# Kernel tuning notes

Measured on AMD Instinct MI355X. Metric: run time of the kernel, lower is better.

Reference implementation:

```python
import jax, jax.numpy as jnp
import numpy as np

B, S, DMODEL = 1, 2048, 4096
H, HKV, DH = 32, 8, 128
LTAB, RBKT = 20, 128
NEG = -1e9


def rotate_half(x):
    x1, x2 = x[..., : x.shape[-1] // 2], x[..., x.shape[-1] // 2:]
    return jnp.concatenate((-x2, x1), axis=-1)


def setup_inputs() -> dict:
    key = jax.random.key(0)
    ks = jax.random.split(key, 12)
    inp = {
        "hidden_states": jax.random.normal(ks[0], (B, S, DMODEL), jnp.float32),
        "cos": jax.random.uniform(ks[1], (B, S, DH), jnp.float32),
        "sin": jax.random.uniform(ks[2], (B, S, DH), jnp.float32),
        "q_probs": jax.random.uniform(ks[3], (B, H, LTAB, RBKT), jnp.float32),
        "v_norm": jax.random.uniform(ks[4], (B, H, S), jnp.float32),
        "allowed": jnp.ones((B, H, S), dtype=bool),
        "k_hard": jax.random.randint(ks[5], (B, H, LTAB, S), 0, RBKT, jnp.int32),
        "Wq": jax.random.normal(ks[6], (DMODEL, H * DH), jnp.float32) * 0.02,
        "Wk": jax.random.normal(ks[7], (DMODEL, HKV * DH), jnp.float32) * 0.02,
        "Wv": jax.random.normal(ks[8], (DMODEL, HKV * DH), jnp.float32) * 0.02,
        "Wo": jax.random.normal(ks[9], (H * DH, DMODEL), jnp.float32) * 0.02,
        "sink": 4,
        "window": 128,
        "M": 256,
    }
    return inp


def _sparse_key_mask(q_probs, v_norm, allowed, k_hard, sink, window, M):
    """Faithful jax version of build_sparse_list_decode, returned as a boolean
    allowed-key mask [B, H, T] (equivalent to scattering sparse_list)."""
    Bm, Hm, _, T = k_hard.shape
    # soft-hash collision score: sum over tables of q bucket prob at key's bucket,
    # weighted by value-norm history, restricted to allowed keys.
    coll = jnp.take_along_axis(q_probs, k_hard.astype(jnp.int32), axis=-1).sum(axis=2)  # [B,H,T]
    scores = jnp.where(allowed, coll * v_norm, -jnp.inf)
    M_eff = min(M, T)
    mask = jnp.zeros((Bm, Hm, T), dtype=bool)
    if M_eff > 0:
        heavy_idx = jax.lax.top_k(scores, M_eff)[1]  # [B,H,M]
        b_ix = jnp.arange(Bm)[:, None, None]
        h_ix = jnp.arange(Hm)[None, :, None]
        mask = mask.at[b_ix, h_ix, heavy_idx].set(True)
    sink = max(0, min(sink, T))
    window = max(0, min(window, T))
    if sink > 0:
        mask = mask.at[:, :, :sink].set(True)
    if window > 0:
        win_start = max(T - window, sink)
        if win_start < T:
            mask = mask.at[:, :, win_start:].set(True)
    if sink == 0 and window == 0:
        mask = mask.at[:, :, T - 1].set(True)
    return mask & allowed


def reference(hidden_states, cos, sin, q_probs, v_norm, allowed, k_hard,
              Wq, Wk, Wv, Wo, sink, window, M):
    Bx, Sx, _ = hidden_states.shape
    scaling = DH ** -0.5
    q = (hidden_states @ Wq).reshape(Bx, Sx, H, DH).transpose(0, 2, 1, 3)   # [B,H,S,Dh]
    k = (hidden_states @ Wk).reshape(Bx, Sx, HKV, DH).transpose(0, 2, 1, 3)  # [B,Hkv,S,Dh]
    v = (hidden_states @ Wv).reshape(Bx, Sx, HKV, DH).transpose(0, 2, 1, 3)
    # RoPE (unsqueeze_dim=1)
    c, s = cos[:, None, :, :], sin[:, None, :, :]
    q = q * c + rotate_half(q) * s
    k = k * c + rotate_half(k) * s
    # repeat_kv for GQA
    n_rep = H // HKV
    k = jnp.repeat(k, n_rep, axis=1)
    v = jnp.repeat(v, n_rep, axis=1)
    # sparse heavy-hitter + sink + window key mask (no_grad in the original)
    key_mask = _sparse_key_mask(q_probs, v_norm, allowed, k_hard, sink, window, M)  # [B,H,S]
    causal = jnp.tril(jnp.ones((Sx, Sx), dtype=bool))
    allow = causal[None, None] & key_mask[:, :, None, :]  # [B,H,S,S]
    scores = jnp.einsum('bhqd,bhkd->bhqk', q, k) * scaling
    attn = jax.nn.softmax(jnp.where(allow, scores, NEG), axis=-1)
    out = jnp.einsum('bhqk,bhkd->bhqd', attn, v)
    out = out.transpose(0, 2, 1, 3).reshape(Bx, Sx, H * DH)
    return out @ Wo
```

## Files before the change

### kernel.cpp

```cpp
#include <hip/hip_runtime.h>
#include <hip/hip_bf16.h>
#include <cstdint>
#include <cstddef>

namespace {

constexpr int S_LEN = 2048;
constexpr int DM    = 4096;
constexpr int NH    = 32;
constexpr int NKV   = 8;
constexpr int DH    = 128;
constexpr int LTAB  = 20;
constexpr int RBKT  = 128;
constexpr int NQKV  = NH * DH + 2 * NKV * DH;
constexpr int KOFF  = NH * DH;
constexpr int VOFF  = NH * DH + NKV * DH;

typedef short s16x8 __attribute__((ext_vector_type(8)));
typedef float f32x4 __attribute__((ext_vector_type(4)));
typedef unsigned long long u64;
struct u64x2 { u64 x, y; };

__device__ inline short bf16s(float f) {
  __hip_bfloat16 b = __float2bfloat16(f);
  return (short)*reinterpret_cast<unsigned short*>(&b);
}
__device__ inline float s2f(short s) {
  unsigned short u = (unsigned short)s;
  return __bfloat162float(*reinterpret_cast<__hip_bfloat16*>(&u));
}

__global__ __launch_bounds__(256) void prep_kernel(
    const float* __restrict__ hidden, const float* __restrict__ Wq,
    const float* __restrict__ Wk, const float* __restrict__ Wv,
    const float* __restrict__ Wo, __hip_bfloat16* __restrict__ hbf,
    __hip_bfloat16* __restrict__ WqkvT, __hip_bfloat16* __restrict__ WoT,
    const float* __restrict__ q_probs, const float* __restrict__ v_norm,
    const int* __restrict__ allowed, const int* __restrict__ k_hard,
    const int* __restrict__ sinkp, const int* __restrict__ winp,
    const int* __restrict__ Mp, int* __restrict__ sel_idx, int* __restrict__ sel_cnt) {
  __shared__ float tile[64][65];
  __shared__ u64 keys[S_LEN];
  __shared__ int waveTot[4];
  const int b = blockIdx.x, tid = threadIdx.x;
  if (b < 32) {
    const int h = b;
    const int lane = tid & 63, wv4 = tid >> 6;
    const int t0 = tid * 8;
    float cs[8] = {0.f, 0.f, 0.f, 0.f, 0.f, 0.f, 0.f, 0.f};
#pragma unroll
    for (int l = 0; l < LTAB; ++l) {
      const int* kb = &k_hard[(size_t)(h * LTAB + l) * S_LEN + t0];
      const int4 ka = *reinterpret_cast<const int4*>(kb);
      const int4 kc = *reinterpret_cast<const int4*>(kb + 4);
      const float* qp = &q_probs[(h * LTAB + l) * RBKT];
      cs[0] += qp[ka.x]; cs[1] += qp[ka.y]; cs[2] += qp[ka.z]; cs[3] += qp[ka.w];
      cs[4] += qp[kc.x]; cs[5] += qp[kc.y]; cs[6] += qp[kc.z]; cs[7] += qp[kc.w];
    }
    const int4 alA = *reinterpret_cast<const int4*>(&allowed[h * S_LEN + t0]);
    const int4 alB = *reinterpret_cast<const int4*>(&allowed[h * S_LEN + t0 + 4]);
    const float4 vnA = *reinterpret_cast<const float4*>(&v_norm[h * S_LEN + t0]);
    const float4 vnB = *reinterpret_cast<const float4*>(&v_norm[h * S_LEN + t0 + 4]);
    const int al[8] = {alA.x, alA.y, alA.z, alA.w, alB.x, alB.y, alB.z, alB.w};
    const float vn[8] = {vnA.x, vnA.y, vnA.z, vnA.w, vnB.x, vnB.y, vnB.z, vnB.w};
    auto mkkey = [](float s, int t) -> u64 {
      unsigned m = __float_as_uint(s);
      m = (m & 0x80000000u) ? ~m : (m | 0x80000000u);
      return ((u64)m << 11) | (u64)(S_LEN - 1 - t);
    };
    u64 kk[8];
#pragma unroll
    for (int c = 0; c < 8; ++c) {
      const float sc = al[c] ? cs[c] * vn[c] : -INFINITY;
      kk[c] = mkkey(sc, t0 + c);
      keys[t0 + c] = kk[c];
    }
    __syncthreads();
    int rk[8] = {0, 0, 0, 0, 0, 0, 0, 0};
#pragma unroll 4
    for (int u = 0; u < S_LEN; u += 2) {
      const u64x2 kv = *reinterpret_cast<const u64x2*>(&keys[u]);
#pragma unroll
      for (int c = 0; c < 8; ++c) rk[c] += (kv.x > kk[c]) + (kv.y > kk[c]);
    }
    const int Mv = min(Mp[0], S_LEN);
    int sv = sinkp[0];
    sv = sv < 0 ? 0 : (sv > S_LEN ? S_LEN : sv);
    int wvv = winp[0];
    wvv = wvv < 0 ? 0 : (wvv > S_LEN ? S_LEN : wvv);
    int wstart = S_LEN - wvv;
    if (wstart < sv) wstart = sv;
    bool sel[8];
    int cnt = 0;
#pragma unroll
    for (int c = 0; c < 8; ++c) {
      const int t = t0 + c;
      bool s = rk[c] < Mv;
      if (t < sv) s = true;
      if (wvv > 0 && t >= wstart) s = true;
      if (sv == 0 && wvv == 0 && t == S_LEN - 1) s = true;
      s = s && (al[c] != 0);
      sel[c] = s;
      cnt += s ? 1 : 0;
    }
    int inc = cnt;
#pragma unroll
    for (int off = 1; off < 64; off <<= 1) {
      int n = __shfl_up(inc, off);
      if (lane >= off) inc += n;
    }
    if (lane == 63) waveTot[wv4] = inc;
    __syncthreads();
    int wbase = 0;
    for (int w = 0; w < wv4; ++w) wbase += waveTot[w];
    int pos = wbase + inc - cnt;
    if (tid == 0) sel_cnt[h] = waveTot[0] + waveTot[1] + waveTot[2] + waveTot[3];
#pragma unroll
    for (int c = 0; c < 8; ++c)
      if (sel[c]) sel_idx[h * S_LEN + pos++] = t0 + c;
    return;
  }
  if (b < 32 + 2048) {
    const size_t base = (size_t)(b - 32) * 1024;
#pragma unroll
    for (int it = 0; it < 4; ++it) {
      const size_t i = base + it * 256 + tid;
      float4 v = reinterpret_cast<const float4*>(hidden)[i];
      ushort4 o;
      o.x = (unsigned short)bf16s(v.x);
      o.y = (unsigned short)bf16s(v.y);
      o.z = (unsigned short)bf16s(v.z);
      o.w = (unsigned short)bf16s(v.w);
      reinterpret_cast<ushort4*>(hbf)[i] = o;
    }
    return;
  }
  const float* W;
  __hip_bfloat16* Wt;
  int N, bx, by;
  int t = b - 2080;
  if (t < 4096) {
    W = Wq; Wt = WqkvT; N = DM; bx = t & 63; by = t >> 6;
  } else if (t < 5120) {
    t -= 4096; W = Wk; Wt = WqkvT + (size_t)KOFF * DM; N = NKV * DH; bx = t & 15; by = t >> 4;
  } else if (t < 6144) {
    t -= 5120; W = Wv; Wt = WqkvT + (size_t)VOFF * DM; N = NKV * DH; bx = t & 15; by = t >> 4;
  } else {
    t -= 6144; W = Wo; Wt = WoT; N = DM; bx = t & 63; by = t >> 6;
  }
  const int K = DM;
  const int kb = by * 64, nb = bx * 64;
  const int r0 = tid >> 4, c4 = (tid & 15) * 4;
#pragma unroll
  for (int it = 0; it < 4; ++it) {
    const int r = r0 + it * 16;
    float4 v = *reinterpret_cast<const float4*>(&W[(size_t)(kb + r) * N + nb + c4]);
    tile[r][c4] = v.x;
    tile[r][c4 + 1] = v.y;
    tile[r][c4 + 2] = v.z;
    tile[r][c4 + 3] = v.w;
  }
  __syncthreads();
  const int n0 = tid >> 4, k4 = (tid & 15) * 4;
#pragma unroll
  for (int it = 0; it < 4; ++it) {
    const int n = n0 + it * 16;
    ushort4 o;
    o.x = (unsigned short)bf16s(tile[k4][n]);
    o.y = (unsigned short)bf16s(tile[k4 + 1][n]);
    o.z = (unsigned short)bf16s(tile[k4 + 2][n]);
    o.w = (unsigned short)bf16s(tile[k4 + 3][n]);
    *reinterpret_cast<ushort4*>(&Wt[(size_t)(nb + n) * K + kb + k4]) = o;
  }
}

template <bool OUT_F32>
__global__ __launch_bounds__(256) void gemm_bt(const __hip_bfloat16* __restrict__ A,
                                               const __hip_bfloat16* __restrict__ Bt,
                                               void* __restrict__ Cout,
                                               int N, int K) {
  __shared__ __hip_bfloat16 As[128 * 64];
  __shared__ __hip_bfloat16 Bs[128 * 64];
  const int tid = threadIdx.x;
  const int wid = tid >> 6;
  const int lane = tid & 63;
  const int bm = blockIdx.y, bn = blockIdx.x;
  const int wr = wid >> 1, wc = wid & 1;
  f32x4 acc[4][4] = {};
  const __hip_bfloat16* Abase = A + (size_t)bm * 128 * K;
  const __hip_bfloat16* Bbase = Bt + (size_t)bn * 128 * K;
  for (int kt = 0; kt < K; kt += 64) {
    __syncthreads();
#pragma unroll
    for (int j = 0; j < 4; ++j) {
      const int pb = j * 4096 + wid * 1024;
      const int p = pb + lane * 16;
      const int row = p >> 7;
      const int slot = ((p >> 4) & 7) ^ (row & 7);
      const int goff = row * K + kt + slot * 8;
      __builtin_amdgcn_global_load_lds(
          (const __attribute__((address_space(1))) void*)(Abase + goff),
          (__attribute__((address_space(3))) void*)(As + (pb >> 1)), 16, 0, 0);
      __builtin_amdgcn_global_load_lds(
          (const __attribute__((address_space(1))) void*)(Bbase + goff),
          (__attribute__((address_space(3))) void*)(Bs + (pb >> 1)), 16, 0, 0);
    }
    __syncthreads();
#pragma unroll
    for (int kk = 0; kk < 2; ++kk) {
      s16x8 af[4], bf[4];
#pragma unroll
      for (int i = 0; i < 4; ++i) {
        const int ra = wr * 64 + i * 16 + (lane & 15);
        const int sa = (kk * 4 + (lane >> 4)) ^ (ra & 7);
        af[i] = *reinterpret_cast<const s16x8*>(As + ra * 64 + sa * 8);
        const int rb = wc * 64 + i * 16 + (lane & 15);
        const int sb = (kk * 4 + (lane >> 4)) ^ (rb & 7);
        bf[i] = *reinterpret_cast<const s16x8*>(Bs + rb * 64 + sb * 8);
      }
#pragma unroll
      for (int i = 0; i < 4; ++i)
#pragma unroll
        for (int jn = 0; jn < 4; ++jn)
          acc[i][jn] = __builtin_amdgcn_mfma_f32_16x16x32_bf16(af[i], bf[jn], acc[i][jn], 0, 0, 0);
    }
  }
  const int rg = (lane >> 4) * 4;
  const int cg = lane & 15;
#pragma unroll
  for (int i = 0; i < 4; ++i)
#pragma unroll
    for (int jn = 0; jn < 4; ++jn)
#pragma unroll
      for (int r = 0; r < 4; ++r) {
        const int rr = bm * 128 + wr * 64 + i * 16 + rg + r;
        const int cc = bn * 128 + wc * 64 + jn * 16 + cg;
        if (OUT_F32)
          reinterpret_cast<float*>(Cout)[(size_t)rr * N + cc] = acc[i][jn][r];
        else
          reinterpret_cast<__hip_bfloat16*>(Cout)[(size_t)rr * N + cc] =
              __float2bfloat16(acc[i][jn][r]);
      }
}

__global__ __launch_bounds__(256) void gemm_bt_splitk(const __hip_bfloat16* __restrict__ A,
                                                      const __hip_bfloat16* __restrict__ Bt,
                                                      float* __restrict__ P,
                                                      int N, int Kfull, int KH) {
  __shared__ __hip_bfloat16 As[128 * 64];
  __shared__ __hip_bfloat16 Bs[128 * 64];
  const int tid = threadIdx.x;
  const int wid = tid >> 6;
  const int lane = tid & 63;
  const int bm = blockIdx.y, bn = blockIdx.x, kz = blockIdx.z;
  const int wr = wid >> 1, wc = wid & 1;
  f32x4 acc[4][4] = {};
  const __hip_bfloat16* Abase = A + (size_t)bm * 128 * Kfull + kz * KH;
  const __hip_bfloat16* Bbase = Bt + (size_t)bn * 128 * Kfull + kz * KH;
  for (int kt = 0; kt < KH; kt += 64) {
    __syncthreads();
#pragma unroll
    for (int j = 0; j < 4; ++j) {
      const int pb = j * 4096 + wid * 1024;
      const int p = pb + lane * 16;
      const int row = p >> 7;
      const int slot = ((p >> 4) & 7) ^ (row & 7);
      const int goff = row * Kfull + kt + slot * 8;
      __builtin_amdgcn_global_load_lds(
          (const __attribute__((address_space(1))) void*)(Abase + goff),
          (__attribute__((address_space(3))) void*)(As + (pb >> 1)), 16, 0, 0);
      __builtin_amdgcn_global_load_lds(
          (const __attribute__((address_space(1))) void*)(Bbase + goff),
          (__attribute__((address_space(3))) void*)(Bs + (pb >> 1)), 16, 0, 0);
    }
    __syncthreads();
#pragma unroll
    for (int kk = 0; kk < 2; ++kk) {
      s16x8 af[4], bf[4];
#pragma unroll
      for (int i = 0; i < 4; ++i) {
        const int ra = wr * 64 + i * 16 + (lane & 15);
        const int sa = (kk * 4 + (lane >> 4)) ^ (ra & 7);
        af[i] = *reinterpret_cast<const s16x8*>(As + ra * 64 + sa * 8);
        const int rb = wc * 64 + i * 16 + (lane & 15);
        const int sb = (kk * 4 + (lane >> 4)) ^ (rb & 7);
        bf[i] = *reinterpret_cast<const s16x8*>(Bs + rb * 64 + sb * 8);
      }
#pragma unroll
      for (int i = 0; i < 4; ++i)
#pragma unroll
        for (int jn = 0; jn < 4; ++jn)
          acc[i][jn] = __builtin_amdgcn_mfma_f32_16x16x32_bf16(af[i], bf[jn], acc[i][jn], 0, 0, 0);
    }
  }
  float* Pz = P + (size_t)kz * S_LEN * N;
  const int rg = (lane >> 4) * 4;
  const int cg = lane & 15;
#pragma unroll
  for (int i = 0; i < 4; ++i)
#pragma unroll
    for (int jn = 0; jn < 4; ++jn)
#pragma unroll
      for (int r = 0; r < 4; ++r) {
        const int rr = bm * 128 + wr * 64 + i * 16 + rg + r;
        const int cc = bn * 128 + wc * 64 + jn * 16 + cg;
        Pz[(size_t)rr * N + cc] = acc[i][jn][r];
      }
}

__global__ __launch_bounds__(256) void reduce_splitk(const float* __restrict__ P,
                                                     float* __restrict__ out, int n4) {
  const int i = blockIdx.x * 256 + threadIdx.x;
  if (i >= n4) return;
  const float4 a = reinterpret_cast<const float4*>(P)[i];
  const float4 b = reinterpret_cast<const float4*>(P + (size_t)S_LEN * DM)[i];
  float4 o;
  o.x = a.x + b.x;
  o.y = a.y + b.y;
  o.z = a.z + b.z;
  o.w = a.w + b.w;
  reinterpret_cast<float4*>(out)[i] = o;
}

__global__ __launch_bounds__(256) void rope_kernel(const __hip_bfloat16* __restrict__ QKV,
                                                   const float* __restrict__ cosb,
                                                   const float* __restrict__ sinb,
                                                   __hip_bfloat16* __restrict__ Qro,
                                                   __hip_bfloat16* __restrict__ Kro) {
  const int s = blockIdx.x;
  const int tid = threadIdx.x;
  const float* cs = cosb + s * DH;
  const float* sn = sinb + s * DH;
  const __hip_bfloat16* row = QKV + (size_t)s * NQKV;
  for (int ch = tid; ch < 512 + 128; ch += 256) {
    const bool isQ = ch < 512;
    const int idx8 = (isQ ? ch : ch - 512) * 8;
    const int d8 = idx8 & (DH - 1);
    const int hb = idx8 - d8;
    const __hip_bfloat16* src = isQ ? row : row + KOFF;
    s16x8 v = *reinterpret_cast<const s16x8*>(src + idx8);
    s16x8 p = *reinterpret_cast<const s16x8*>(src + hb + (d8 ^ 64));
    const float sgn = (d8 < 64) ? -1.f : 1.f;
    s16x8 outv;
#pragma unroll
    for (int j = 0; j < 8; ++j) {
      const float r = s2f(v[j]) * cs[d8 + j] + sgn * s2f(p[j]) * sn[d8 + j];
      outv[j] = bf16s(r);
    }
    if (isQ)
      *reinterpret_cast<s16x8*>(Qro + (size_t)s * (NH * DH) + idx8) = outv;
    else
      *reinterpret_cast<s16x8*>(Kro + (size_t)s * (NKV * DH) + idx8) = outv;
  }
}

__global__ __launch_bounds__(256) void attn_kernel(const __hip_bfloat16* __restrict__ Qro,
                                                   const __hip_bfloat16* __restrict__ Kro,
                                                   const __hip_bfloat16* __restrict__ Vpk,
                                                   const int* __restrict__ sel_idx,
                                                   const int* __restrict__ sel_cnt,
                                                   __hip_bfloat16* __restrict__ ctx) {
  constexpr int BKV = 64;
  const int h = blockIdx.y;
  const int q0 = blockIdx.x * 64;
  const int tid = threadIdx.x, wid = tid >> 6, lane = tid & 63;
  const int l15 = lane & 15, hi = lane >> 4;
  const int kv = h >> 2;
  __shared__ __hip_bfloat16 Ks[BKV][DH + 8];
  __shared__ __hip_bfloat16 Vt[DH][BKV + 8];
  __shared__ __hip_bfloat16 Ps[4][16][BKV + 8];
  __shared__ int tIdx[BKV];
  const int qbase = q0 + wid * 16;
  const float scaling = 0.08838834764831845f;
  s16x8 qf[4];
  {
    const __hip_bfloat16* qp =
        Qro + (size_t)(qbase + l15) * (NH * DH) + h * DH + hi * 8;
#pragma unroll
    for (int kt = 0; kt < 4; ++kt) {
      s16x8 q = *reinterpret_cast<const s16x8*>(qp + kt * 32);
#pragma unroll
      for (int j = 0; j < 8; ++j) q[j] = bf16s(s2f(q[j]) * scaling);
      qf[kt] = q;
    }
  }
  s16x8 ones;
#pragma unroll
  for (int j = 0; j < 8; ++j) ones[j] = (short)0x3F80;
  float mr[4], lr[4];
#pragma unroll
  for (int r = 0; r < 4; ++r) {
    mr[r] = -3.0e38f;
    lr[r] = 0.f;
  }
  f32x4 o[8] = {};
  const int cnt = sel_cnt[h];
  const int qmax = q0 + 63;
  for (int j0 = 0; j0 < cnt; j0 += BKV) {
    if (sel_idx[h * S_LEN + j0] > qmax) break;
    const int nk = min(BKV, cnt - j0);
    __syncthreads();
    if (tid < BKV) tIdx[tid] = (tid < nk) ? sel_idx[h * S_LEN + j0 + tid] : 0x7fffffff;
#pragma unroll
    for (int c = 0; c < 4; ++c) {
      const int ch = tid + c * 256;
      const int row = ch >> 4, c8 = ch & 15;
      if (row < nk) {
        const int t = sel_idx[h * S_LEN + j0 + row];
        *reinterpret_cast<s16x8*>(&Ks[row][c8 * 8]) = *reinterpret_cast<const s16x8*>(
            Kro + (size_t)t * (NKV * DH) + kv * DH + c8 * 8);
      }
    }
    {
      const int j = tid >> 2;
      const int dp = (tid & 3) * 32;
      const int ccA = j ^ (((dp >> 4) & 7) << 3);
      const int ccB = j ^ ((((dp >> 4) + 1) & 7) << 3);
      if (j < nk) {
        const int t = sel_idx[h * S_LEN + j0 + j];
        const __hip_bfloat16* vp = Vpk + (size_t)t * NQKV + kv * DH + dp;
        s16x8 a = *reinterpret_cast<const s16x8*>(vp);
        s16x8 bq = *reinterpret_cast<const s16x8*>(vp + 8);
        s16x8 cq = *reinterpret_cast<const s16x8*>(vp + 16);
        s16x8 dq = *reinterpret_cast<const s16x8*>(vp + 24);
#pragma unroll
        for (int i = 0; i < 8; ++i) reinterpret_cast<short&>(Vt[dp + i][ccA]) = a[i];
#pragma unroll
        for (int i = 0; i < 8; ++i) reinterpret_cast<short&>(Vt[dp + 8 + i][ccA]) = bq[i];
#pragma unroll
        for (int i = 0; i < 8; ++i) reinterpret_cast<short&>(Vt[dp + 16 + i][ccB]) = cq[i];
#pragma unroll
        for (int i = 0; i < 8; ++i) reinterpret_cast<short&>(Vt[dp + 24 + i][ccB]) = dq[i];
      } else {
#pragma unroll
        for (int i = 0; i < 16; ++i) reinterpret_cast<short&>(Vt[dp + i][ccA]) = 0;
#pragma unroll
        for (int i = 0; i < 16; ++i) reinterpret_cast<short&>(Vt[dp + 16 + i][ccB]) = 0;
      }
    }
    __syncthreads();
    f32x4 sc[4];
#pragma unroll
    for (int kc = 0; kc < 4; ++kc) sc[kc] = f32x4{0.f, 0.f, 0.f, 0.f};
#pragma unroll
    for (int kt = 0; kt < 4; ++kt) {
#pragma unroll
      for (int kc = 0; kc < 4; ++kc) {
        const s16x8 kf =
            *reinterpret_cast<const s16x8*>(&Ks[kc * 16 + l15][kt * 32 + hi * 8]);
        sc[kc] = __builtin_amdgcn_mfma_f32_16x16x32_bf16(qf[kt], kf, sc[kc], 0, 0, 0);
      }
    }
    int tt[4];
#pragma unroll
    for (int kc = 0; kc < 4; ++kc) tt[kc] = tIdx[kc * 16 + l15];
    float vv[4][4];
    bool need = false;
#pragma unroll
    for (int r = 0; r < 4; ++r) {
      const int qs = qbase + (hi << 2) + r;
      float mx = -3.0e38f;
#pragma unroll
      for (int kc = 0; kc < 4; ++kc) {
        vv[kc][r] = (tt[kc] <= qs) ? sc[kc][r] : -1.0e9f;
        mx = fmaxf(mx, vv[kc][r]);
      }
      need = need || (mx > mr[r] + 8.f);
    }
    if (__any(need)) {
#pragma unroll
      for (int r = 0; r < 4; ++r) {
        float m = fmaxf(fmaxf(vv[0][r], vv[1][r]), fmaxf(vv[2][r], vv[3][r]));
#pragma unroll
        for (int off = 1; off < 16; off <<= 1) m = fmaxf(m, __shfl_xor(m, off));
        const float mn = fmaxf(mr[r], m);
        const float scl = __expf(mr[r] - mn);
        lr[r] *= scl;
#pragma unroll
        for (int nt = 0; nt < 8; ++nt) o[nt][r] *= scl;
        mr[r] = mn;
      }
    }
#pragma unroll
    for (int r = 0; r < 4; ++r) {
#pragma unroll
      for (int kc = 0; kc < 4; ++kc) {
        Ps[wid][(hi << 2) + r][kc * 16 + l15] = __float2bfloat16(__expf(vv[kc][r] - mr[r]));
      }
    }
    const s16x8 pf0 = *reinterpret_cast<const s16x8*>(&Ps[wid][l15][hi * 8]);
    const s16x8 pf1 = *reinterpret_cast<const s16x8*>(&Ps[wid][l15][32 + hi * 8]);
    {
      f32x4 zero = {0.f, 0.f, 0.f, 0.f};
      f32x4 ps = __builtin_amdgcn_mfma_f32_16x16x32_bf16(pf0, ones, zero, 0, 0, 0);
      ps = __builtin_amdgcn_mfma_f32_16x16x32_bf16(pf1, ones, ps, 0, 0, 0);
#pragma unroll
      for (int r = 0; r < 4; ++r) lr[r] += ps[r];
    }
#pragma unroll
    for (int nt = 0; nt < 8; ++nt) {
      const s16x8 vfa =
          *reinterpret_cast<const s16x8*>(&Vt[nt * 16 + l15][(hi * 8) ^ (nt * 8)]);
      const s16x8 vfb =
          *reinterpret_cast<const s16x8*>(&Vt[nt * 16 + l15][(32 + hi * 8) ^ (nt * 8)]);
      o[nt] = __builtin_amdgcn_mfma_f32_16x16x32_bf16(pf0, vfa, o[nt], 0, 0, 0);
      o[nt] = __builtin_amdgcn_mfma_f32_16x16x32_bf16(pf1, vfb, o[nt], 0, 0, 0);
    }
  }
#pragma unroll
  for (int nt = 0; nt < 8; ++nt)
#pragma unroll
    for (int r = 0; r < 4; ++r) {
      const int qs = qbase + (hi << 2) + r;
      const int d = nt * 16 + l15;
      ctx[(size_t)qs * (NH * DH) + h * DH + d] = __float2bfloat16(o[nt][r] / lr[r]);
    }
}

}

extern "C" void kernel_launch(void* const* d_in, const int* in_sizes, int n_in,
                              void* d_out, int out_size, void* d_ws, size_t ws_size,
                              hipStream_t stream) {
  const float* hidden = (const float*)d_in[0];
  const float* cosb = (const float*)d_in[1];
  const float* sinb = (const float*)d_in[2];
  const float* q_probs = (const float*)d_in[3];
  const float* v_norm = (const float*)d_in[4];
  const int* allowed = (const int*)d_in[5];
  const int* k_hard = (const int*)d_in[6];
  const float* Wq = (const float*)d_in[7];
  const float* Wk = (const float*)d_in[8];
  const float* Wv = (const float*)d_in[9];
  const float* Wo = (const float*)d_in[10];
  const int* sinkp = (const int*)d_in[11];
  const int* winp = (const int*)d_in[12];
  const int* Mp = (const int*)d_in[13];

  char* ws = (char*)d_ws;
  size_t off = 0;
  auto alloc = [&](size_t bytes) -> char* {
    char* p = ws + off;
    off += (bytes + 255) & ~(size_t)255;
    return p;
  };
  __hip_bfloat16* hbf = (__hip_bfloat16*)alloc((size_t)S_LEN * DM * 2);
  __hip_bfloat16* WqkvT = (__hip_bfloat16*)alloc((size_t)NQKV * DM * 2);
  __hip_bfloat16* WoT = (__hip_bfloat16*)alloc((size_t)DM * DM * 2);
  __hip_bfloat16* QKV = (__hip_bfloat16*)alloc((size_t)S_LEN * NQKV * 2);
  __hip_bfloat16* Qro = (__hip_bfloat16*)alloc((size_t)S_LEN * NH * DH * 2);
  __hip_bfloat16* Kro = (__hip_bfloat16*)alloc((size_t)S_LEN * NKV * DH * 2);
  __hip_bfloat16* ctx = (__hip_bfloat16*)alloc((size_t)S_LEN * NH * DH * 2);
  int* sel_idx = (int*)alloc((size_t)NH * S_LEN * 4);
  int* sel_cnt = (int*)alloc((size_t)NH * 4);
  if (off > ws_size) return;
  float* Psplit = (float*)hbf;

  prep_kernel<<<12320, 256, 0, stream>>>(hidden, Wq, Wk, Wv, Wo, hbf, WqkvT, WoT, q_probs,
                                         v_norm, allowed, k_hard, sinkp, winp, Mp, sel_idx,
                                         sel_cnt);

  gemm_bt<false><<<dim3(NQKV / 128, S_LEN / 128), 256, 0, stream>>>(
      hbf, WqkvT, (void*)QKV, NQKV, DM);

  rope_kernel<<<S_LEN, 256, 0, stream>>>(QKV, cosb, sinb, Qro, Kro);

  attn_kernel<<<dim3(S_LEN / 64, NH), 256, 0, stream>>>(Qro, Kro, QKV + VOFF, sel_idx,
                                                        sel_cnt, ctx);

  gemm_bt_splitk<<<dim3(DM / 128, S_LEN / 128, 2), 256, 0, stream>>>(ctx, WoT, Psplit, DM,
                                                                     DM, DM / 2);
  reduce_splitk<<<(S_LEN * DM / 4 + 255) / 256, 256, 0, stream>>>((const float*)Psplit,
                                                                  (float*)d_out,
                                                                  S_LEN * DM / 4);
}
```

Baseline: 385.6 us.

## Move Wo transpose into the QKV GEMM launch to overlap with compute

The fp32-to-bf16 transpose of Wo is taken out of the prep kernel and run as extra workgroups appended to the QKV projection GEMM grid, which is now a 1D launch. The memory-bound transpose can then overlap with the compute-bound GEMM instead of serializing ahead of it, and the prep kernel becomes shorter. Shared memory is merged into a raw buffer in both kernels. The risk is that transpose blocks scheduled at the grid tail extend the GEMM's runtime, or that they compete with the GEMM for bandwidth.

```diff
diff --git a/kernel.cpp b/kernel.cpp
--- a/kernel.cpp
+++ b/kernel.cpp
@@ -15,6 +15,7 @@
 constexpr int NQKV  = NH * DH + 2 * NKV * DH;
 constexpr int KOFF  = NH * DH;
 constexpr int VOFF  = NH * DH + NKV * DH;
+constexpr int QKV_NWG = (S_LEN / 128) * (NQKV / 128);
 
 typedef short s16x8 __attribute__((ext_vector_type(8)));
 typedef float f32x4 __attribute__((ext_vector_type(4)));
@@ -30,20 +31,47 @@
   return __bfloat162float(*reinterpret_cast<__hip_bfloat16*>(&u));
 }
 
+__device__ inline void transpose64_body(const float* __restrict__ W,
+                                        __hip_bfloat16* __restrict__ Wt, int N, int bx,
+                                        int by, int tid, float (*tile)[65]) {
+  const int kb = by * 64, nb = bx * 64;
+  const int r0 = tid >> 4, c4 = (tid & 15) * 4;
+#pragma unroll
+  for (int it = 0; it < 4; ++it) {
+    const int r = r0 + it * 16;
+    float4 v = *reinterpret_cast<const float4*>(&W[(size_t)(kb + r) * N + nb + c4]);
+    tile[r][c4] = v.x;
+    tile[r][c4 + 1] = v.y;
+    tile[r][c4 + 2] = v.z;
+    tile[r][c4 + 3] = v.w;
+  }
+  __syncthreads();
+  const int n0 = tid >> 4, k4 = (tid & 15) * 4;
+#pragma unroll
+  for (int it = 0; it < 4; ++it) {
+    const int n = n0 + it * 16;
+    ushort4 o;
+    o.x = (unsigned short)bf16s(tile[k4][n]);
+    o.y = (unsigned short)bf16s(tile[k4 + 1][n]);
+    o.z = (unsigned short)bf16s(tile[k4 + 2][n]);
+    o.w = (unsigned short)bf16s(tile[k4 + 3][n]);
+    *reinterpret_cast<ushort4*>(&Wt[(size_t)(nb + n) * DM + kb + k4]) = o;
+  }
+}
+
 __global__ __launch_bounds__(256) void prep_kernel(
     const float* __restrict__ hidden, const float* __restrict__ Wq,
     const float* __restrict__ Wk, const float* __restrict__ Wv,
-    const float* __restrict__ Wo, __hip_bfloat16* __restrict__ hbf,
-    __hip_bfloat16* __restrict__ WqkvT, __hip_bfloat16* __restrict__ WoT,
+    __hip_bfloat16* __restrict__ hbf, __hip_bfloat16* __restrict__ WqkvT,
     const float* __restrict__ q_probs, const float* __restrict__ v_norm,
     const int* __restrict__ allowed, const int* __restrict__ k_hard,
     const int* __restrict__ sinkp, const int* __restrict__ winp,
     const int* __restrict__ Mp, int* __restrict__ sel_idx, int* __restrict__ sel_cnt) {
-  __shared__ float tile[64][65];
-  __shared__ u64 keys[S_LEN];
+  __shared__ __align__(16) char smem[64 * 65 * 4];
   __shared__ int waveTot[4];
   const int b = blockIdx.x, tid = threadIdx.x;
   if (b < 32) {
+    u64* keys = reinterpret_cast<u64*>(smem);
     const int h = b;
     const int lane = tid & 63, wv4 = tid >> 6;
     const int t0 = tid * 8;
@@ -135,6 +163,7 @@
     }
     return;
   }
+  float (*tile)[65] = reinterpret_cast<float(*)[65]>(smem);
   const float* W;
   __hip_bfloat16* Wt;
   int N, bx, by;
@@ -143,48 +172,31 @@
     W = Wq; Wt = WqkvT; N = DM; bx = t & 63; by = t >> 6;
   } else if (t < 5120) {
     t -= 4096; W = Wk; Wt = WqkvT + (size_t)KOFF * DM; N = NKV * DH; bx = t & 15; by = t >> 4;
-  } else if (t < 6144) {
+  } else {
     t -= 5120; W = Wv; Wt = WqkvT + (size_t)VOFF * DM; N = NKV * DH; bx = t & 15; by = t >> 4;
-  } else {
-    t -= 6144; W = Wo; Wt = WoT; N = DM; bx = t & 63; by = t >> 6;
-  }
-  const int K = DM;
-  const int kb = by * 64, nb = bx * 64;
-  const int r0 = tid >> 4, c4 = (tid & 15) * 4;
-#pragma unroll
-  for (int it = 0; it < 4; ++it) {
-    const int r = r0 + it * 16;
-    float4 v = *reinterpret_cast<const float4*>(&W[(size_t)(kb + r) * N + nb + c4]);
-    tile[r][c4] = v.x;
-    tile[r][c4 + 1] = v.y;
-    tile[r][c4 + 2] = v.z;
-    tile[r][c4 + 3] = v.w;
-  }
-  __syncthreads();
-  const int n0 = tid >> 4, k4 = (tid & 15) * 4;
-#pragma unroll
-  for (int it = 0; it < 4; ++it) {
-    const int n = n0 + it * 16;
-    ushort4 o;
-    o.x = (unsigned short)bf16s(tile[k4][n]);
-    o.y = (unsigned short)bf16s(tile[k4 + 1][n]);
-    o.z = (unsigned short)bf16s(tile[k4 + 2][n]);
-    o.w = (unsigned short)bf16s(tile[k4 + 3][n]);
-    *reinterpret_cast<ushort4*>(&Wt[(size_t)(nb + n) * K + kb + k4]) = o;
-  }
-}
-
-template <bool OUT_F32>
-__global__ __launch_bounds__(256) void gemm_bt(const __hip_bfloat16* __restrict__ A,
-                                               const __hip_bfloat16* __restrict__ Bt,
-                                               void* __restrict__ Cout,
-                                               int N, int K) {
-  __shared__ __hip_bfloat16 As[128 * 64];
-  __shared__ __hip_bfloat16 Bs[128 * 64];
-  const int tid = threadIdx.x;
+  }
+  transpose64_body(W, Wt, N, bx, by, tid, tile);
+}
+
+__global__ __launch_bounds__(256) void gemm_qkv_wo(const __hip_bfloat16* __restrict__ A,
+                                                   const __hip_bfloat16* __restrict__ Bt,
+                                                   __hip_bfloat16* __restrict__ Cout,
+                                                   const float* __restrict__ Wo,
+                                                   __hip_bfloat16* __restrict__ WoT) {
+  __shared__ __align__(16) char smem[128 * 64 * 2 * 2];
+  const int bid = blockIdx.x, tid = threadIdx.x;
+  if (bid >= QKV_NWG) {
+    float (*tile)[65] = reinterpret_cast<float(*)[65]>(smem);
+    const int t = bid - QKV_NWG;
+    transpose64_body(Wo, WoT, DM, t & 63, t >> 6, tid, tile);
+    return;
+  }
+  __hip_bfloat16* As = reinterpret_cast<__hip_bfloat16*>(smem);
+  __hip_bfloat16* Bs = As + 128 * 64;
+  constexpr int N = NQKV, K = DM;
+  const int bn = bid % (NQKV / 128), bm = bid / (NQKV / 128);
   const int wid = tid >> 6;
   const int lane = tid & 63;
-  const int bm = blockIdx.y, bn = blockIdx.x;
   const int wr = wid >> 1, wc = wid & 1;
   f32x4 acc[4][4] = {};
   const __hip_bfloat16* Abase = A + (size_t)bm * 128 * K;
@@ -235,11 +247,7 @@
       for (int r = 0; r < 4; ++r) {
         const int rr = bm * 128 + wr * 64 + i * 16 + rg + r;
         const int cc = bn * 128 + wc * 64 + jn * 16 + cg;
-        if (OUT_F32)
-          reinterpret_cast<float*>(Cout)[(size_t)rr * N + cc] = acc[i][jn][r];
-        else
-          reinterpret_cast<__hip_bfloat16*>(Cout)[(size_t)rr * N + cc] =
-              __float2bfloat16(acc[i][jn][r]);
+        Cout[(size_t)rr * N + cc] = __float2bfloat16(acc[i][jn][r]);
       }
 }
 
@@ -556,12 +564,10 @@
   if (off > ws_size) return;
   float* Psplit = (float*)hbf;
 
-  prep_kernel<<<12320, 256, 0, stream>>>(hidden, Wq, Wk, Wv, Wo, hbf, WqkvT, WoT, q_probs,
-                                         v_norm, allowed, k_hard, sinkp, winp, Mp, sel_idx,
-                                         sel_cnt);
-
-  gemm_bt<false><<<dim3(NQKV / 128, S_LEN / 128), 256, 0, stream>>>(
-      hbf, WqkvT, (void*)QKV, NQKV, DM);
+  prep_kernel<<<8224, 256, 0, stream>>>(hidden, Wq, Wk, Wv, hbf, WqkvT, q_probs, v_norm,
+                                        allowed, k_hard, sinkp, winp, Mp, sel_idx, sel_cnt);
+
+  gemm_qkv_wo<<<QKV_NWG + 4096, 256, 0, stream>>>(hbf, WqkvT, QKV, Wo, WoT);
 
   rope_kernel<<<S_LEN, 256, 0, stream>>>(QKV, cosb, sinb, Qro, Kro);
 
```

Measured after the change: 420.1 us. 1.09x slower.
